# Kernel tuning notes

Hardware: AMD Instinct MI355X
Metric: run time of the kernel (lower is better)

The kernel has to match this reference:

```python
import jax, jax.numpy as jnp
import numpy as np

NB = 8  # num_blocks

def setup_inputs() -> dict:
    key = jax.random.key(0)
    ks = jax.random.split(key, 8)
    C = 128
    C8 = C // 8
    s = 0.05
    x = jax.random.normal(ks[0], (1, C, 64, 64, 64), dtype=jnp.float32)
    Wq = jax.random.normal(ks[1], (C8, C), dtype=jnp.float32) * s
    bq = jax.random.normal(ks[2], (C8,), dtype=jnp.float32) * s
    Wk = jax.random.normal(ks[3], (C8, C), dtype=jnp.float32) * s
    bk = jax.random.normal(ks[4], (C8,), dtype=jnp.float32) * s
    Wv = jax.random.normal(ks[5], (C, C), dtype=jnp.float32) * s
    bv = jax.random.normal(ks[6], (C,), dtype=jnp.float32) * s
    # torch inits gamma=0 (output == x, zero grads through attention);
    # use 0.5 so the attention path is actually exercised.
    gamma = jnp.full((1,), 0.5, dtype=jnp.float32)
    return dict(x=x, Wq=Wq, bq=bq, Wk=Wk, bk=bk, Wv=Wv, bv=bv, gamma=gamma)

def reference(x, Wq, bq, Wk, bk, Wv, bv, gamma):
    B, C, D, H, W = x.shape
    db, hb, wb = D // NB, H // NB, W // NB
    n = db * hb * wb
    # (i, j, k, B, C, db, hb, wb) block layout
    xr = x.reshape(B, C, NB, db, NB, hb, NB, wb).transpose(2, 4, 6, 0, 1, 3, 5, 7)
    ar = jnp.arange(NB)
    # NOTE: original code computes k = i % num_blocks, i.e. k == i always.
    # Only the (i, j, i) diagonal blocks are attended; the rest stay zero in `out`.
    blk = xr[ar, :, ar].reshape(NB * NB * B, C, n)  # (P, C, n), P = NB*NB*B
    # 1x1x1 convs == per-voxel linear layers over channels
    q = jnp.einsum('pcn,dc->pdn', blk, Wq) + bq[None, :, None]  # (P, C/8, n)
    k = jnp.einsum('pcn,dc->pdn', blk, Wk) + bk[None, :, None]  # (P, C/8, n)
    v = jnp.einsum('pcn,dc->pdn', blk, Wv) + bv[None, :, None]  # (P, C,   n)
    attn = jax.nn.softmax(jnp.einsum('pdn,pdm->pnm', q, k), axis=-1)  # (P, n_q, n_k)
    ob = jnp.einsum('pdm,pnm->pdn', v, attn)  # value @ attn^T, (P, C, n)
    ob = ob.reshape(NB, NB, B, C, db, hb, wb)
    out = jnp.zeros_like(xr).at[ar, :, ar].set(ob)  # only k==i diagonal filled
    out = out.transpose(3, 4, 0, 5, 1, 6, 2, 7).reshape(B, C, D, H, W)
    return gamma * out + x
```

## Files before the change

### kernel.cpp

```cpp
#include <hip/hip_runtime.h>

typedef __attribute__((ext_vector_type(8))) short bf16x8;
typedef __attribute__((ext_vector_type(4))) float f32x4;
typedef __attribute__((ext_vector_type(4))) int i32x4;
typedef __attribute__((ext_vector_type(4))) float float4v;

#define MFMA16(a, b, c) __builtin_amdgcn_mfma_f32_16x16x32_bf16((a), (b), (c), 0, 0, 0)

__device__ __forceinline__ unsigned short f2bf(float f) {
    unsigned u = __builtin_bit_cast(unsigned, f);
    u += 0x7fffu + ((u >> 16) & 1u);
    return (unsigned short)(u >> 16);
}
__device__ __forceinline__ float bf2f(unsigned short s) {
    unsigned u = ((unsigned)s) << 16;
    return __builtin_bit_cast(float, u);
}
__device__ __forceinline__ int pkbf(float a, float b) {
    return (int)f2bf(a) | ((int)f2bf(b) << 16);
}

#define KOFF 131072
#define LOFF 147456

__global__ __launch_bounds__(512, 2) void battn_kernel(
    const float* __restrict__ x,
    const float* __restrict__ Wq, const float* __restrict__ bq,
    const float* __restrict__ Wk, const float* __restrict__ bk,
    const float* __restrict__ Wv, const float* __restrict__ bv,
    const float* __restrict__ gamma, float* __restrict__ out)
{
    __shared__ __attribute__((aligned(128))) char smem[149504];
    const int bid = blockIdx.x;
    const int tid = threadIdx.x;

    if (bid >= 64) {
        const float4v* __restrict__ xin = (const float4v*)x;
        float4v* __restrict__ o4 = (float4v*)out;
        const int total = 1 << 23;
        const int T = (int)((gridDim.x - 64) << 9);
        int u = ((bid - 64) << 9) + tid;
#define PRED(v) (((((v) >> 1) ^ ((v) >> 13)) & 7) != 0)
        for (; u + 3 * T < total; u += 4 * T) {
            float4v a0 = xin[u];
            float4v a1 = xin[u + T];
            float4v a2 = xin[u + 2 * T];
            float4v a3 = xin[u + 3 * T];
            if (PRED(u)) o4[u] = a0;
            if (PRED(u + T)) o4[u + T] = a1;
            if (PRED(u + 2 * T)) o4[u + 2 * T] = a2;
            if (PRED(u + 3 * T)) o4[u + 3 * T] = a3;
        }
        for (; u < total; u += T)
            if (PRED(u)) o4[u] = xin[u];
#undef PRED
        return;
    }

    const int p = bid;
    const int ib = p >> 3, jb = p & 7;
    const int vbase = ib * 8 * 4096 + jb * 8 * 64 + ib * 8;
    const int lane = tid & 63, wv = tid >> 6;
    const int g = lane >> 4, c15 = lane & 15;

    for (int it = 0; it < 32; ++it) {
        int ch = it * 512 + tid;
        int c = ch >> 7;
        int m = (ch & 127) * 4;
        int vox = ((m >> 6) << 12) + (((m >> 3) & 7) << 6) + (m & 7);
        float4v v = *(const float4v*)(x + c * 262144 + vbase + vox);
        char* bp = smem + ((m * 256 + 2 * c) ^ (((m >> 2) & 7) << 4));
        *(unsigned short*)(bp)       = f2bf(v[0]);
        *(unsigned short*)(bp + 256) = f2bf(v[1]);
        *(unsigned short*)(bp + 512) = f2bf(v[2]);
        *(unsigned short*)(bp + 768) = f2bf(v[3]);
    }

    bf16x8 wqf[4], wkf[4], wvf[4];
    #pragma unroll
    for (int ks = 0; ks < 4; ++ks) {
        const float* sq = Wq + c15 * 128 + ks * 32 + g * 8;
        const float* sk = Wk + c15 * 128 + ks * 32 + g * 8;
        const float* sv = Wv + (wv * 16 + c15) * 128 + ks * 32 + g * 8;
        #pragma unroll
        for (int e = 0; e < 8; ++e) {
            wqf[ks][e] = (short)f2bf(sq[e]);
            wkf[ks][e] = (short)f2bf(sk[e]);
            wvf[ks][e] = (short)f2bf(sv[e]);
        }
    }
    const float bqv = bq[c15], bkv = bk[c15];
    const f32x4 zacc = {0.f, 0.f, 0.f, 0.f};
    const bf16x8 zfrag = (bf16x8)(short)0;

    __syncthreads();

    #pragma unroll
    for (int qi = 0; qi < 4; ++qi) {
        f32x4 acc = zacc;
        int mrow = wv * 64 + qi * 16 + c15;
        int sw = ((mrow >> 2) & 7) << 4;
        #pragma unroll
        for (int ks = 0; ks < 4; ++ks) {
            bf16x8 af = *(const bf16x8*)(smem + ((mrow * 256 + ks * 64 + g * 16) ^ sw));
            acc = MFMA16(af, wqf[ks], acc);
        }
        #pragma unroll
        for (int r = 0; r < 4; ++r) {
            int nql = qi * 16 + g * 4 + r;
            *(unsigned short*)(smem + KOFF + wv * 2048 + nql * 32 + 2 * c15) = f2bf(acc[r] + bqv);
        }
    }
    bf16x8 qf[4];
    #pragma unroll
    for (int t = 0; t < 4; ++t) {
        bf16x8 v = zfrag;
        if (g < 2) v = *(const bf16x8*)(smem + KOFF + wv * 2048 + (t * 16 + c15) * 32 + g * 16);
        qf[t] = v;
    }

    #pragma unroll
    for (int qi = 0; qi < 4; ++qi) {
        f32x4 acc = zacc;
        int mrow = wv * 64 + qi * 16 + c15;
        int sw = ((mrow >> 2) & 7) << 4;
        #pragma unroll
        for (int ks = 0; ks < 4; ++ks) {
            bf16x8 af = *(const bf16x8*)(smem + ((mrow * 256 + ks * 64 + g * 16) ^ sw));
            acc = MFMA16(af, wkf[ks], acc);
        }
        #pragma unroll
        for (int r = 0; r < 4; ++r) {
            int mk = wv * 64 + qi * 16 + g * 4 + r;
            *(unsigned short*)(smem + KOFF + mk * 32 + 2 * c15) = f2bf(acc[r] + bkv);
        }
    }

    f32x4 vacc[32];
    #pragma unroll
    for (int mt = 0; mt < 32; ++mt) vacc[mt] = zacc;
    #pragma unroll
    for (int mt = 0; mt < 32; ++mt) {
        int mrow = mt * 16 + c15;
        int sw = ((mrow >> 2) & 7) << 4;
        #pragma unroll
        for (int ks = 0; ks < 4; ++ks) {
            bf16x8 bf = *(const bf16x8*)(smem + ((mrow * 256 + ks * 64 + g * 16) ^ sw));
            vacc[mt] = MFMA16(wvf[ks], bf, vacc[mt]);
        }
    }
    __syncthreads();

    #pragma unroll
    for (int mt = 0; mt < 32; ++mt) {
        #pragma unroll
        for (int r = 0; r < 4; ++r) {
            int c_out = wv * 16 + g * 4 + r;
            int mk = mt * 16 + c15;
            *(unsigned short*)(smem + c_out * 1024 + ((2 * mk) ^ ((c_out & 7) << 4))) = f2bf(vacc[mt][r]);
        }
    }
    __syncthreads();

    f32x4 o[4][8];
    #pragma unroll
    for (int t = 0; t < 4; ++t)
        #pragma unroll
        for (int ci = 0; ci < 8; ++ci)
            o[t][ci] = zacc;
    float lsum[4] = {0.f, 0.f, 0.f, 0.f};

    for (int kt = 0; kt < 16; ++kt) {
        int mk0 = kt * 32;
        bf16x8 ka[2];
        #pragma unroll
        for (int ki = 0; ki < 2; ++ki) {
            bf16x8 v = zfrag;
            if (g < 2) v = *(const bf16x8*)(smem + KOFF + (mk0 + ki * 16 + c15) * 32 + g * 16);
            ka[ki] = v;
        }

        bf16x8 pa[4];
        #pragma unroll
        for (int t = 0; t < 4; ++t) {
            f32x4 s0 = MFMA16(ka[0], qf[t], zacc);
            f32x4 s1 = MFMA16(ka[1], qf[t], zacc);
            float e00 = __expf(s0[0]), e01 = __expf(s0[1]), e02 = __expf(s0[2]), e03 = __expf(s0[3]);
            float e10 = __expf(s1[0]), e11 = __expf(s1[1]), e12 = __expf(s1[2]), e13 = __expf(s1[3]);
            lsum[t] += (e00 + e01) + (e02 + e03) + ((e10 + e11) + (e12 + e13));
            int wA0 = pkbf(e00, e01), wB0 = pkbf(e02, e03);
            int wA1 = pkbf(e10, e11), wB1 = pkbf(e12, e13);
            int src1 = ((2 * g) & 3) * 16 + c15;
            int src2 = ((2 * g + 1) & 3) * 16 + c15;
            int sA0a = __shfl(wA0, src1, 64), sA1a = __shfl(wA1, src1, 64);
            int sB0a = __shfl(wB0, src1, 64), sB1a = __shfl(wB1, src1, 64);
            int sA0b = __shfl(wA0, src2, 64), sA1b = __shfl(wA1, src2, 64);
            int sB0b = __shfl(wB0, src2, 64), sB1b = __shfl(wB1, src2, 64);
            bool k1 = (g >= 2);
            i32x4 uu = { k1 ? sA1a : sA0a, k1 ? sB1a : sB0a,
                         k1 ? sA1b : sA0b, k1 ? sB1b : sB0b };
            pa[t] = __builtin_bit_cast(bf16x8, uu);
        }

        #pragma unroll
        for (int ci = 0; ci < 8; ++ci) {
            int c = ci * 16 + c15;
            bf16x8 vb = *(const bf16x8*)(smem + c * 1024 + ((mk0 * 2 + 16 * g) ^ ((c & 7) << 4)));
            #pragma unroll
            for (int t = 0; t < 4; ++t)
                o[t][ci] = MFMA16(pa[t], vb, o[t][ci]);
        }
    }

    #pragma unroll
    for (int t = 0; t < 4; ++t) {
        float l = lsum[t];
        l += __shfl_xor(l, 16, 64);
        l += __shfl_xor(l, 32, 64);
        if (g == 0)
            *(float*)(smem + LOFF + (wv * 64 + t * 16 + c15) * 4) = l;
    }

    __syncthreads();

    #pragma unroll
    for (int t = 0; t < 4; ++t)
        #pragma unroll
        for (int ci = 0; ci < 8; ++ci)
            #pragma unroll
            for (int r = 0; r < 4; ++r) {
                int nq = wv * 64 + t * 16 + g * 4 + r;
                int c = ci * 16 + c15;
                *(unsigned short*)(smem + c * 1024 + ((2 * nq) ^ ((c & 7) << 4))) = f2bf(o[t][ci][r]);
            }
    __syncthreads();

    float gma = gamma[0];
    float invl = 1.0f / *(const float*)(smem + LOFF + tid * 4);
    int vox = ((tid >> 6) << 12) + (((tid >> 3) & 7) << 6) + (tid & 7);
    int go = vbase + vox;
    for (int c = 0; c < 128; ++c) {
        float ov = bf2f(*(const unsigned short*)(smem + c * 1024 + ((2 * tid) ^ ((c & 7) << 4))));
        int gidx = c * 262144 + go;
        out[gidx] = gma * (ov * invl + bv[c]) + x[gidx];
    }
}

extern "C" void kernel_launch(void* const* d_in, const int* in_sizes, int n_in,
                              void* d_out, int out_size, void* d_ws, size_t ws_size,
                              hipStream_t stream) {
    const float* x     = (const float*)d_in[0];
    const float* Wq    = (const float*)d_in[1];
    const float* bq    = (const float*)d_in[2];
    const float* Wk    = (const float*)d_in[3];
    const float* bk    = (const float*)d_in[4];
    const float* Wv    = (const float*)d_in[5];
    const float* bv    = (const float*)d_in[6];
    const float* gamma = (const float*)d_in[7];
    float* out = (float*)d_out;
    (void)in_sizes; (void)n_in; (void)out_size; (void)d_ws; (void)ws_size;
    battn_kernel<<<dim3(512), dim3(512), 0, stream>>>(x, Wq, bq, Wk, bk, Wv, bv, gamma, out);
}
```

Before: 110.8 us.

## Split residual copy into separate kernel and batch global loads in attention kernel

Moves the off-diagonal residual copy out of the fused kernel into a dedicated copy kernel with 256-thread blocks. The attention kernel now launches only 64 blocks and runs after the copy on the same stream instead of alongside it. The attention kernel also batches its global loads (8 float4 loads in flight before the bf16 conversion, vectorized weight loads, 8 batched x loads in the epilogue). The V projection is chunked into four 128-voxel pieces to reduce register pressure. The risk is that serializing the two kernels loses the overlap of the copy with the attention compute, which the fused grid previously provided.

```diff
diff --git a/kernel.cpp b/kernel.cpp
--- a/kernel.cpp
+++ b/kernel.cpp
@@ -18,6 +18,27 @@
 }
 __device__ __forceinline__ int pkbf(float a, float b) {
     return (int)f2bf(a) | ((int)f2bf(b) << 16);
+}
+
+__global__ __launch_bounds__(256, 8) void copy_kernel(
+    const float4v* __restrict__ xin, float4v* __restrict__ o4)
+{
+    const int S = 2048 * 256;
+    int u = blockIdx.x * 256 + threadIdx.x;
+#define PRED(v) (((((v) >> 1) ^ ((v) >> 13)) & 7) != 0)
+    #pragma unroll
+    for (int i = 0; i < 4; ++i) {
+        float4v a0 = xin[u];
+        float4v a1 = xin[u + S];
+        float4v a2 = xin[u + 2 * S];
+        float4v a3 = xin[u + 3 * S];
+        if (PRED(u)) o4[u] = a0;
+        if (PRED(u + S)) o4[u + S] = a1;
+        if (PRED(u + 2 * S)) o4[u + 2 * S] = a2;
+        if (PRED(u + 3 * S)) o4[u + 3 * S] = a3;
+        u += 4 * S;
+    }
+#undef PRED
 }
 
 #define KOFF 131072
@@ -31,62 +52,51 @@
     const float* __restrict__ gamma, float* __restrict__ out)
 {
     __shared__ __attribute__((aligned(128))) char smem[149504];
-    const int bid = blockIdx.x;
     const int tid = threadIdx.x;
-
-    if (bid >= 64) {
-        const float4v* __restrict__ xin = (const float4v*)x;
-        float4v* __restrict__ o4 = (float4v*)out;
-        const int total = 1 << 23;
-        const int T = (int)((gridDim.x - 64) << 9);
-        int u = ((bid - 64) << 9) + tid;
-#define PRED(v) (((((v) >> 1) ^ ((v) >> 13)) & 7) != 0)
-        for (; u + 3 * T < total; u += 4 * T) {
-            float4v a0 = xin[u];
-            float4v a1 = xin[u + T];
-            float4v a2 = xin[u + 2 * T];
-            float4v a3 = xin[u + 3 * T];
-            if (PRED(u)) o4[u] = a0;
-            if (PRED(u + T)) o4[u + T] = a1;
-            if (PRED(u + 2 * T)) o4[u + 2 * T] = a2;
-            if (PRED(u + 3 * T)) o4[u + 3 * T] = a3;
-        }
-        for (; u < total; u += T)
-            if (PRED(u)) o4[u] = xin[u];
-#undef PRED
-        return;
-    }
-
-    const int p = bid;
+    const int p = blockIdx.x;
     const int ib = p >> 3, jb = p & 7;
     const int vbase = ib * 8 * 4096 + jb * 8 * 64 + ib * 8;
     const int lane = tid & 63, wv = tid >> 6;
     const int g = lane >> 4, c15 = lane & 15;
 
-    for (int it = 0; it < 32; ++it) {
-        int ch = it * 512 + tid;
-        int c = ch >> 7;
-        int m = (ch & 127) * 4;
-        int vox = ((m >> 6) << 12) + (((m >> 3) & 7) << 6) + (m & 7);
-        float4v v = *(const float4v*)(x + c * 262144 + vbase + vox);
-        char* bp = smem + ((m * 256 + 2 * c) ^ (((m >> 2) & 7) << 4));
-        *(unsigned short*)(bp)       = f2bf(v[0]);
-        *(unsigned short*)(bp + 256) = f2bf(v[1]);
-        *(unsigned short*)(bp + 512) = f2bf(v[2]);
-        *(unsigned short*)(bp + 768) = f2bf(v[3]);
+    #pragma unroll
+    for (int b = 0; b < 4; ++b) {
+        float4v t[8];
+        #pragma unroll
+        for (int j = 0; j < 8; ++j) {
+            int ch = (b * 8 + j) * 512 + tid;
+            int c = ch >> 7;
+            int m = (ch & 127) * 4;
+            int vox = ((m >> 6) << 12) + (((m >> 3) & 7) << 6) + (m & 7);
+            t[j] = *(const float4v*)(x + c * 262144 + vbase + vox);
+        }
+        #pragma unroll
+        for (int j = 0; j < 8; ++j) {
+            int ch = (b * 8 + j) * 512 + tid;
+            int c = ch >> 7;
+            int m = (ch & 127) * 4;
+            char* bp = smem + ((m * 256 + 2 * c) ^ (((m >> 2) & 7) << 4));
+            *(unsigned short*)(bp)       = f2bf(t[j][0]);
+            *(unsigned short*)(bp + 256) = f2bf(t[j][1]);
+            *(unsigned short*)(bp + 512) = f2bf(t[j][2]);
+            *(unsigned short*)(bp + 768) = f2bf(t[j][3]);
+        }
     }
 
     bf16x8 wqf[4], wkf[4], wvf[4];
     #pragma unroll
     for (int ks = 0; ks < 4; ++ks) {
-        const float* sq = Wq + c15 * 128 + ks * 32 + g * 8;
-        const float* sk = Wk + c15 * 128 + ks * 32 + g * 8;
-        const float* sv = Wv + (wv * 16 + c15) * 128 + ks * 32 + g * 8;
-        #pragma unroll
-        for (int e = 0; e < 8; ++e) {
-            wqf[ks][e] = (short)f2bf(sq[e]);
-            wkf[ks][e] = (short)f2bf(sk[e]);
-            wvf[ks][e] = (short)f2bf(sv[e]);
+        const float4v* sq = (const float4v*)(Wq + c15 * 128 + ks * 32 + g * 8);
+        const float4v* sk = (const float4v*)(Wk + c15 * 128 + ks * 32 + g * 8);
+        const float4v* sv = (const float4v*)(Wv + (wv * 16 + c15) * 128 + ks * 32 + g * 8);
+        float4v q0 = sq[0], q1 = sq[1];
+        float4v k0 = sk[0], k1 = sk[1];
+        float4v v0 = sv[0], v1 = sv[1];
+        #pragma unroll
+        for (int e = 0; e < 4; ++e) {
+            wqf[ks][e] = (short)f2bf(q0[e]); wqf[ks][4 + e] = (short)f2bf(q1[e]);
+            wkf[ks][e] = (short)f2bf(k0[e]); wkf[ks][4 + e] = (short)f2bf(k1[e]);
+            wvf[ks][e] = (short)f2bf(v0[e]); wvf[ks][4 + e] = (short)f2bf(v1[e]);
         }
     }
     const float bqv = bq[c15], bkv = bk[c15];
@@ -136,28 +146,29 @@
         }
     }
 
-    f32x4 vacc[32];
-    #pragma unroll
-    for (int mt = 0; mt < 32; ++mt) vacc[mt] = zacc;
-    #pragma unroll
-    for (int mt = 0; mt < 32; ++mt) {
-        int mrow = mt * 16 + c15;
-        int sw = ((mrow >> 2) & 7) << 4;
-        #pragma unroll
-        for (int ks = 0; ks < 4; ++ks) {
-            bf16x8 bf = *(const bf16x8*)(smem + ((mrow * 256 + ks * 64 + g * 16) ^ sw));
-            vacc[mt] = MFMA16(wvf[ks], bf, vacc[mt]);
-        }
-    }
-    __syncthreads();
-
-    #pragma unroll
-    for (int mt = 0; mt < 32; ++mt) {
-        #pragma unroll
-        for (int r = 0; r < 4; ++r) {
-            int c_out = wv * 16 + g * 4 + r;
-            int mk = mt * 16 + c15;
-            *(unsigned short*)(smem + c_out * 1024 + ((2 * mk) ^ ((c_out & 7) << 4))) = f2bf(vacc[mt][r]);
+    for (int ck = 0; ck < 4; ++ck) {
+        f32x4 vacc[8];
+        #pragma unroll
+        for (int mt = 0; mt < 8; ++mt) {
+            vacc[mt] = zacc;
+            int mrow = ck * 128 + mt * 16 + c15;
+            int sw = ((mrow >> 2) & 7) << 4;
+            #pragma unroll
+            for (int ks = 0; ks < 4; ++ks) {
+                bf16x8 bf = *(const bf16x8*)(smem + ((mrow * 256 + ks * 64 + g * 16) ^ sw));
+                vacc[mt] = MFMA16(wvf[ks], bf, vacc[mt]);
+            }
+        }
+        __syncthreads();
+        #pragma unroll
+        for (int mt = 0; mt < 8; ++mt) {
+            #pragma unroll
+            for (int r = 0; r < 4; ++r) {
+                int c_out = wv * 16 + g * 4 + r;
+                int mkl = mt * 16 + c15;
+                *(unsigned short*)(smem + ck * 32768 + c_out * 256 +
+                                   ((2 * mkl) ^ ((c_out & 7) << 4))) = f2bf(vacc[mt][r]);
+            }
         }
     }
     __syncthreads();
@@ -202,10 +213,12 @@
             pa[t] = __builtin_bit_cast(bf16x8, uu);
         }
 
+        int ckbase = (mk0 >> 7) * 32768;
+        int mklb = (2 * (mk0 & 127)) + 16 * g;
         #pragma unroll
         for (int ci = 0; ci < 8; ++ci) {
             int c = ci * 16 + c15;
-            bf16x8 vb = *(const bf16x8*)(smem + c * 1024 + ((mk0 * 2 + 16 * g) ^ ((c & 7) << 4)));
+            bf16x8 vb = *(const bf16x8*)(smem + ckbase + c * 256 + (mklb ^ ((c & 7) << 4)));
             #pragma unroll
             for (int t = 0; t < 4; ++t)
                 o[t][ci] = MFMA16(pa[t], vb, o[t][ci]);
@@ -239,10 +252,17 @@
     float invl = 1.0f / *(const float*)(smem + LOFF + tid * 4);
     int vox = ((tid >> 6) << 12) + (((tid >> 3) & 7) << 6) + (tid & 7);
     int go = vbase + vox;
-    for (int c = 0; c < 128; ++c) {
-        float ov = bf2f(*(const unsigned short*)(smem + c * 1024 + ((2 * tid) ^ ((c & 7) << 4))));
-        int gidx = c * 262144 + go;
-        out[gidx] = gma * (ov * invl + bv[c]) + x[gidx];
+    for (int cb = 0; cb < 16; ++cb) {
+        float xv[8];
+        #pragma unroll
+        for (int j = 0; j < 8; ++j)
+            xv[j] = x[(cb * 8 + j) * 262144 + go];
+        #pragma unroll
+        for (int j = 0; j < 8; ++j) {
+            int c = cb * 8 + j;
+            float ov = bf2f(*(const unsigned short*)(smem + c * 1024 + ((2 * tid) ^ ((c & 7) << 4))));
+            out[c * 262144 + go] = gma * (ov * invl + bv[c]) + xv[j];
+        }
     }
 }
 
@@ -259,5 +279,6 @@
     const float* gamma = (const float*)d_in[7];
     float* out = (float*)d_out;
     (void)in_sizes; (void)n_in; (void)out_size; (void)d_ws; (void)ws_size;
-    battn_kernel<<<dim3(512), dim3(512), 0, stream>>>(x, Wq, bq, Wk, bk, Wv, bv, gamma, out);
-}
+    copy_kernel<<<dim3(2048), dim3(256), 0, stream>>>((const float4v*)x, (float4v*)out);
+    battn_kernel<<<dim3(64), dim3(512), 0, stream>>>(x, Wq, bq, Wk, bk, Wv, bv, gamma, out);
+}
```

After: 131.2 us. 18.4% more time.
